# Performance work log

Hardware: AMD Instinct MI355X
Metric: run time of the kernel (lower is better)

The kernel has to match this reference:

```python
import jax, jax.numpy as jnp
import numpy as np

BATCH = 8192          # per-modality batch size; n = 2*BATCH
FEAT = 128            # feature dim (kept small -> memory-bound n^2 distance matrix)
NUM_IDS = 1000
MARGIN = 0.3


def setup_inputs() -> dict:
    key = jax.random.key(0)
    k1, k2 = jax.random.split(key)
    n = 2 * BATCH
    inputs = jax.random.normal(k1, (n, FEAT), dtype=jnp.float32)
    # same identity set in both modality halves -> cross-modal positives exist per row
    t = jax.random.randint(k2, (BATCH,), 0, NUM_IDS, dtype=jnp.int32)
    targets = jnp.concatenate([t, t], axis=0)
    return {"inputs": inputs, "targets": targets}


def reference(inputs, targets):
    n = inputs.shape[0]
    # pairwise euclidean distances: ||xi||^2 + ||xj||^2 - 2 xi.xj
    sq = jnp.sum(inputs * inputs, axis=1)                      # [n]
    d2 = sq[:, None] + sq[None, :] - 2.0 * (inputs @ inputs.T)  # [n, n]
    dist = jnp.sqrt(jnp.clip(d2, 1e-12, None))
    # modality: first half 0, second half 1; self.sub selects CROSS-modality pairs
    modality = jnp.arange(n) >= (n // 2)
    cross = modality[:, None] != modality[None, :]              # [n, n] bool
    same = targets[:, None] == targets[None, :]                 # same identity
    pos = same & cross        # mask1: same label, different modality
    neg = (~same) & cross     # mask2: diff label, different modality
    # masked hard mining: per-row max over positives, min over negatives
    dist_ap = jnp.max(jnp.where(pos, dist, -jnp.inf), axis=1)   # [n]
    dist_an = jnp.min(jnp.where(neg, dist, jnp.inf), axis=1)    # [n]
    # MarginRankingLoss with y=1: mean(relu(-(dist_an - dist_ap) + margin))
    loss = jnp.mean(jax.nn.relu(dist_ap - dist_an + MARGIN))
    correct = jnp.sum(dist_an >= dist_ap).astype(jnp.int32)
    return (loss, correct)
```

## Files before the change

kernel.cpp:

```cpp
#include <hip/hip_runtime.h>

#define N_TOTAL 16384
#define HALF    8192
#define FEAT    128
#define MARGIN  0.3f
#define NBINS   1024

typedef __attribute__((ext_vector_type(8))) short  short8v;
typedef __attribute__((ext_vector_type(4))) float  float4v;

__device__ __forceinline__ unsigned short f32_to_bf16_rne(float f) {
    unsigned u = __float_as_uint(f);
    u += 0x7FFFu + ((u >> 16) & 1u);
    return (unsigned short)(u >> 16);
}

template<int CTRL>
__device__ __forceinline__ float dpp_mov_f(float x) {
    return __int_as_float(__builtin_amdgcn_update_dpp(
        0, __float_as_int(x), CTRL, 0xF, 0xF, true));
}
__device__ __forceinline__ float rowmin16(float x) {
    x = fminf(x, dpp_mov_f<0xB1>(x));
    x = fminf(x, dpp_mov_f<0x4E>(x));
    x = fminf(x, dpp_mov_f<0x141>(x));
    x = fminf(x, dpp_mov_f<0x140>(x));
    return x;
}
__device__ __forceinline__ float rowmax16(float x) {
    x = fmaxf(x, dpp_mov_f<0xB1>(x));
    x = fmaxf(x, dpp_mov_f<0x4E>(x));
    x = fmaxf(x, dpp_mov_f<0x141>(x));
    x = fmaxf(x, dpp_mov_f<0x140>(x));
    return x;
}

__global__ __launch_bounds__(1024) void histscan_kernel(
        const int* __restrict__ targets, int* __restrict__ cursor,
        int* __restrict__ accs ) {
    __shared__ int lhist[NBINS];
    const int h = blockIdx.x;
    const int t = threadIdx.x;
    lhist[t] = 0;
    __syncthreads();
    const int* tg = targets + (h << 13);
    #pragma unroll
    for (int k = 0; k < 8; ++k)
        atomicAdd(&lhist[tg[k * 1024 + t]], 1);
    __syncthreads();
    const int lane = t & 63, wave = t >> 6;
    int x = lhist[t];
    const int orig = x;
    #pragma unroll
    for (int m = 1; m < 64; m <<= 1) {
        int v = __shfl_up(x, m, 64);
        if (lane >= m) x += v;
    }
    __shared__ int wsum[16];
    if (lane == 63) wsum[wave] = x;
    __syncthreads();
    if (t == 0) {
        int s = 0;
        for (int w = 0; w < 16; ++w) { int v = wsum[w]; wsum[w] = s; s += v; }
        if (h == 0) { accs[0] = 0; accs[1] = 0; accs[2] = 0; }
    }
    __syncthreads();
    cursor[(h << 10) + t] = x - orig + wsum[wave];
}

__global__ __launch_bounds__(256) void prep_kernel(
        const float* __restrict__ X, const int* __restrict__ targets,
        int* __restrict__ cursor,
        unsigned* __restrict__ Xb, float* __restrict__ sq, int* __restrict__ labs) {
    const int wave = threadIdx.x >> 6, lane = threadIdx.x & 63;
    const int src = blockIdx.x * 4 + wave;
    const int h   = src >> 13;
    const int lbl = targets[src];
    int dst;
    if (lane == 0)
        dst = (h << 13) + atomicAdd(&cursor[(h << 10) + lbl], 1);
    dst = __shfl(dst, 0, 64);
    const float2 xv = ((const float2*)(X + (size_t)src * FEAT))[lane];
    unsigned short h0 = f32_to_bf16_rne(xv.x);
    unsigned short h1 = f32_to_bf16_rne(xv.y);
    Xb[dst * 64 + lane] = (unsigned)h0 | ((unsigned)h1 << 16);
    float x0 = __uint_as_float((unsigned)h0 << 16);
    float x1 = __uint_as_float((unsigned)h1 << 16);
    float p = x0 * x0 + x1 * x1;
    #pragma unroll
    for (int m = 1; m < 64; m <<= 1) p += __shfl_xor(p, m, 64);
    if (lane == 0) {
        sq[dst]   = p;
        labs[dst] = lbl;
    }
}

__global__ __launch_bounds__(256, 2) void cross_kernel(
        const unsigned short* __restrict__ Xb, const float* __restrict__ sq,
        const int* __restrict__ labs,
        float* __restrict__ prow_min, float* __restrict__ prow_max,
        float* __restrict__ pcol_min, float* __restrict__ pcol_max) {
    __shared__ unsigned short As[128 * 128];
    __shared__ unsigned short Bs[128 * 128];
    const int bm = blockIdx.x, bn = blockIdx.y;
    const int t  = threadIdx.x;

    const unsigned short* Ag = Xb + (size_t)bm * 128 * FEAT;
    const unsigned short* Bg = Xb + (size_t)(HALF + bn * 128) * FEAT;
    #pragma unroll
    for (int p = 0; p < 8; ++p) {
        int idx = p * 256 + t;
        int row = idx >> 4, ch = idx & 15;
        int sc  = ch ^ (row & 7);
        uint4 va = ((const uint4*)Ag)[idx];
        uint4 vb = ((const uint4*)Bg)[idx];
        *(uint4*)&As[row * 128 + sc * 8] = va;
        *(uint4*)&Bs[row * 128 + sc * 8] = vb;
    }
    __syncthreads();

    const int wave = t >> 6, lane = t & 63;
    const int q = lane >> 4, c = lane & 15;
    const int wr = (wave >> 1) * 64, wc = (wave & 1) * 64;

    float4v acc[4][4] = {};
    #pragma unroll
    for (int kk = 0; kk < 4; ++kk) {
        short8v af[4], bfr[4];
        #pragma unroll
        for (int ti = 0; ti < 4; ++ti) {
            int row = wr + ti * 16 + c;
            int sc  = (kk * 4 + q) ^ (row & 7);
            af[ti] = *(const short8v*)&As[row * 128 + sc * 8];
        }
        #pragma unroll
        for (int tj = 0; tj < 4; ++tj) {
            int row = wc + tj * 16 + c;
            int sc  = (kk * 4 + q) ^ (row & 7);
            bfr[tj] = *(const short8v*)&Bs[row * 128 + sc * 8];
        }
        #pragma unroll
        for (int ti = 0; ti < 4; ++ti)
            #pragma unroll
            for (int tj = 0; tj < 4; ++tj)
                acc[ti][tj] = __builtin_amdgcn_mfma_f32_16x16x32_bf16(
                    af[ti], bfr[tj], acc[ti][tj], 0, 0, 0);
    }

    const float NEG_INF = __int_as_float((int)0xFF800000u);
    const float POS_INF = __int_as_float(0x7F800000);

    const int aMin = labs[bm * 128], aMax = labs[bm * 128 + 127];
    const int bMn  = labs[HALF + bn * 128], bMx = labs[HALF + bn * 128 + 127];
    const bool overlap = (aMax >= bMn) && (bMx >= aMin);

    float sA[16];
    #pragma unroll
    for (int ti = 0; ti < 4; ++ti)
        #pragma unroll
        for (int reg = 0; reg < 4; ++reg)
            sA[ti * 4 + reg] = sq[bm * 128 + wr + ti * 16 + q * 4 + reg];
    float sB[4];
    #pragma unroll
    for (int tj = 0; tj < 4; ++tj)
        sB[tj] = sq[HALF + bn * 128 + wc + tj * 16 + c];

    float rmin[16], rmax[16], cmin[4], cmax[4];
    #pragma unroll
    for (int i = 0; i < 16; ++i) { rmin[i] = POS_INF; rmax[i] = NEG_INF; }
    #pragma unroll
    for (int j = 0; j < 4; ++j)  { cmin[j] = POS_INF; cmax[j] = NEG_INF; }

    if (!overlap) {
        #pragma unroll
        for (int ti = 0; ti < 4; ++ti)
            #pragma unroll
            for (int tj = 0; tj < 4; ++tj)
                #pragma unroll
                for (int reg = 0; reg < 4; ++reg) {
                    int ri = ti * 4 + reg;
                    float d2 = fmaf(acc[ti][tj][reg], -2.0f, sA[ri] + sB[tj]);
                    rmin[ri] = fminf(rmin[ri], d2);
                    cmin[tj] = fminf(cmin[tj], d2);
                }
    } else {
        int tA[16];
        #pragma unroll
        for (int ti = 0; ti < 4; ++ti)
            #pragma unroll
            for (int reg = 0; reg < 4; ++reg)
                tA[ti * 4 + reg] = labs[bm * 128 + wr + ti * 16 + q * 4 + reg];
        int tB[4];
        #pragma unroll
        for (int tj = 0; tj < 4; ++tj)
            tB[tj] = labs[HALF + bn * 128 + wc + tj * 16 + c];

        #pragma unroll
        for (int ti = 0; ti < 4; ++ti)
            #pragma unroll
            for (int tj = 0; tj < 4; ++tj)
                #pragma unroll
                for (int reg = 0; reg < 4; ++reg) {
                    int ri = ti * 4 + reg;
                    float d2 = fmaf(acc[ti][tj][reg], -2.0f, sA[ri] + sB[tj]);
                    bool same = (tA[ri] == tB[tj]);
                    rmin[ri] = fminf(rmin[ri], same ? POS_INF : d2);
                    rmax[ri] = fmaxf(rmax[ri], same ? d2 : NEG_INF);
                    cmin[tj] = fminf(cmin[tj], same ? POS_INF : d2);
                    cmax[tj] = fmaxf(cmax[tj], same ? d2 : NEG_INF);
                }
    }

    #pragma unroll
    for (int i = 0; i < 16; ++i) {
        rmin[i] = rowmin16(rmin[i]);
        rmax[i] = rowmax16(rmax[i]);
    }
    if (c == 0) {
        const int sR = bn * 2 + (wave & 1);
        #pragma unroll
        for (int ti = 0; ti < 4; ++ti)
            #pragma unroll
            for (int reg = 0; reg < 4; ++reg) {
                int gr = bm * 128 + wr + ti * 16 + q * 4 + reg;
                prow_min[sR * HALF + gr] = rmin[ti * 4 + reg];
                prow_max[sR * HALF + gr] = rmax[ti * 4 + reg];
            }
    }

    #pragma unroll
    for (int m = 16; m <= 32; m <<= 1)
        #pragma unroll
        for (int j = 0; j < 4; ++j) {
            cmin[j] = fminf(cmin[j], __shfl_xor(cmin[j], m, 64));
            cmax[j] = fmaxf(cmax[j], __shfl_xor(cmax[j], m, 64));
        }
    if (q == 0) {
        const int sC = bm * 2 + (wave >> 1);
        #pragma unroll
        for (int tj = 0; tj < 4; ++tj) {
            int gc = bn * 128 + wc + tj * 16 + c;
            pcol_min[sC * HALF + gc] = cmin[tj];
            pcol_max[sC * HALF + gc] = cmax[tj];
        }
    }
}

__global__ __launch_bounds__(256) void final_kernel(
        const float* __restrict__ prow_min, const float* __restrict__ prow_max,
        const float* __restrict__ pcol_min, const float* __restrict__ pcol_max,
        int* __restrict__ accs ,
        float* __restrict__ out) {
    const int i = blockIdx.x * 256 + threadIdx.x;
    const int t = threadIdx.x;
    float* accF = (float*)&accs[0];
    int*   accI = &accs[1];
    int*   tick = &accs[2];

    const float* pmn = (i < HALF) ? prow_min : pcol_min;
    const float* pmx = (i < HALF) ? prow_max : pcol_max;
    const int    li  = (i < HALF) ? i : i - HALF;
    float an2 = pmn[li], ap2 = pmx[li];
    #pragma unroll 8
    for (int p = 1; p < 128; ++p) {
        an2 = fminf(an2, pmn[p * HALF + li]);
        ap2 = fmaxf(ap2, pmx[p * HALF + li]);
    }
    float ap = sqrtf(fmaxf(ap2, 1e-12f));
    float an = sqrtf(fmaxf(an2, 1e-12f));
    float term = fmaxf(ap - an + MARGIN, 0.0f);
    int cnt = (an >= ap) ? 1 : 0;
    #pragma unroll
    for (int m = 1; m < 64; m <<= 1) {
        term += __shfl_xor(term, m, 64);
        cnt  += __shfl_xor(cnt, m, 64);
    }
    __shared__ float sf[4];
    __shared__ int   si[4];
    if ((t & 63) == 0) { sf[t >> 6] = term; si[t >> 6] = cnt; }
    __syncthreads();
    if (t == 0) {
        atomicAdd(accF, sf[0] + sf[1] + sf[2] + sf[3]);
        atomicAdd(accI, si[0] + si[1] + si[2] + si[3]);
        __threadfence();
        int old = atomicAdd(tick, 1);
        if (old == gridDim.x - 1) {
            __threadfence();
            float S = atomicAdd(accF, 0.0f);
            int   C = atomicAdd(accI, 0);
            out[0] = S / (float)N_TOTAL;
            out[1] = (float)C;
        }
    }
}

extern "C" void kernel_launch(void* const* d_in, const int* in_sizes, int n_in,
                              void* d_out, int out_size, void* d_ws, size_t ws_size,
                              hipStream_t stream) {
    const float* X       = (const float*)d_in[0];
    const int*   targets = (const int*)d_in[1];
    float* out = (float*)d_out;

    char* ws = (char*)d_ws;
    const size_t XB_BYTES = (size_t)N_TOTAL * FEAT * 2;
    unsigned* Xb    = (unsigned*)ws;
    float* sq       = (float*)(ws + XB_BYTES);
    int* labs       = (int*)(ws + XB_BYTES + 65536);
    char* p         = ws + XB_BYTES + 2 * 65536;
    float* prow_min = (float*)p;  p += 128 * HALF * 4;
    float* prow_max = (float*)p;  p += 128 * HALF * 4;
    float* pcol_min = (float*)p;  p += 128 * HALF * 4;
    float* pcol_max = (float*)p;  p += 128 * HALF * 4;
    int* cursor     = (int*)p;    p += 2 * NBINS * 4;
    int* accs       = (int*)p;

    histscan_kernel<<<2, 1024, 0, stream>>>(targets, cursor, accs);
    prep_kernel    <<<4096, 256, 0, stream>>>(X, targets, cursor, Xb, sq, labs);
    cross_kernel   <<<dim3(64, 64), 256, 0, stream>>>(
        (const unsigned short*)Xb, sq, labs, prow_min, prow_max, pcol_min, pcol_max);
    final_kernel   <<<64, 256, 0, stream>>>(
        prow_min, prow_max, pcol_min, pcol_max, accs, out);
}
```

Before: 132.2 us.

## Pre-swizzle bf16 layout in prep and load tiles via direct global-to-LDS

The prep kernel now writes the bf16 feature matrix in a 16-row blocked layout that matches the MFMA fragment access pattern. The cross kernel then fills shared memory with global_load_lds DMA instructions instead of going through registers with an XOR swizzle. Fragment reads also become simple strided offsets. The aim is to cut register staging and address math in the tile load, but the new layout has to stay consistent with every other consumer of Xb.

```diff
diff --git a/kernel.cpp b/kernel.cpp
--- a/kernel.cpp
+++ b/kernel.cpp
@@ -83,7 +83,8 @@
     const float2 xv = ((const float2*)(X + (size_t)src * FEAT))[lane];
     unsigned short h0 = f32_to_bf16_rne(xv.x);
     unsigned short h1 = f32_to_bf16_rne(xv.y);
-    Xb[dst * 64 + lane] = (unsigned)h0 | ((unsigned)h1 << 16);
+    Xb[(dst >> 4) * 1024 + (lane >> 2) * 64 + (dst & 15) * 4 + (lane & 3)] =
+        (unsigned)h0 | ((unsigned)h1 << 16);
     float x0 = __uint_as_float((unsigned)h0 << 16);
     float x1 = __uint_as_float((unsigned)h1 << 16);
     float p = x0 * x0 + x1 * x1;
@@ -100,45 +101,45 @@
         const int* __restrict__ labs,
         float* __restrict__ prow_min, float* __restrict__ prow_max,
         float* __restrict__ pcol_min, float* __restrict__ pcol_max) {
-    __shared__ unsigned short As[128 * 128];
-    __shared__ unsigned short Bs[128 * 128];
+    __shared__ char Tile[65536];
     const int bm = blockIdx.x, bn = blockIdx.y;
     const int t  = threadIdx.x;
-
-    const unsigned short* Ag = Xb + (size_t)bm * 128 * FEAT;
-    const unsigned short* Bg = Xb + (size_t)(HALF + bn * 128) * FEAT;
-    #pragma unroll
-    for (int p = 0; p < 8; ++p) {
-        int idx = p * 256 + t;
-        int row = idx >> 4, ch = idx & 15;
-        int sc  = ch ^ (row & 7);
-        uint4 va = ((const uint4*)Ag)[idx];
-        uint4 vb = ((const uint4*)Bg)[idx];
-        *(uint4*)&As[row * 128 + sc * 8] = va;
-        *(uint4*)&Bs[row * 128 + sc * 8] = vb;
-    }
-    __syncthreads();
-
     const int wave = t >> 6, lane = t & 63;
+
+    const char* Ag = (const char*)Xb + (size_t)(bm * 8) * 4096;
+    const char* Bg = (const char*)Xb + (size_t)(512 + bn * 8) * 4096;
+    {
+        const int off0 = wave * 8192 + lane * 16;
+        #pragma unroll
+        for (int j = 0; j < 8; ++j) {
+            __builtin_amdgcn_global_load_lds(
+                (const __attribute__((address_space(1))) void*)(Ag + off0 + j * 1024),
+                (__attribute__((address_space(3))) void*)(Tile + off0 + j * 1024),
+                16, 0, 0);
+            __builtin_amdgcn_global_load_lds(
+                (const __attribute__((address_space(1))) void*)(Bg + off0 + j * 1024),
+                (__attribute__((address_space(3))) void*)(Tile + 32768 + off0 + j * 1024),
+                16, 0, 0);
+        }
+    }
+    __syncthreads();
+
     const int q = lane >> 4, c = lane & 15;
     const int wr = (wave >> 1) * 64, wc = (wave & 1) * 64;
 
+    const char* Abase = Tile + (wr >> 4) * 4096 + q * 256 + c * 16;
+    const char* Bbase = Tile + 32768 + (wc >> 4) * 4096 + q * 256 + c * 16;
+
     float4v acc[4][4] = {};
     #pragma unroll
     for (int kk = 0; kk < 4; ++kk) {
         short8v af[4], bfr[4];
         #pragma unroll
-        for (int ti = 0; ti < 4; ++ti) {
-            int row = wr + ti * 16 + c;
-            int sc  = (kk * 4 + q) ^ (row & 7);
-            af[ti] = *(const short8v*)&As[row * 128 + sc * 8];
-        }
-        #pragma unroll
-        for (int tj = 0; tj < 4; ++tj) {
-            int row = wc + tj * 16 + c;
-            int sc  = (kk * 4 + q) ^ (row & 7);
-            bfr[tj] = *(const short8v*)&Bs[row * 128 + sc * 8];
-        }
+        for (int ti = 0; ti < 4; ++ti)
+            af[ti] = *(const short8v*)(Abase + ti * 4096 + kk * 1024);
+        #pragma unroll
+        for (int tj = 0; tj < 4; ++tj)
+            bfr[tj] = *(const short8v*)(Bbase + tj * 4096 + kk * 1024);
         #pragma unroll
         for (int ti = 0; ti < 4; ++ti)
             #pragma unroll
```

After: 133.6 us. Within noise of the previous version (+1.1%).
